# Optimization experiments

Measured on AMD Instinct MI355X. Metric: run time of the kernel, lower is better.

## Reference

```python
import jax, jax.numpy as jnp
import numpy as np

N, E = 20000, 320000
EPS = 1e-5
NEG_SLOPE = 0.2


def gat_conv(x, src, dst, W, att_src, att_dst, bias, num_nodes):
    # W: [Fin, H*C], att_*: [H, C], bias: [H*C]
    H, C = att_src.shape
    h = (x @ W).reshape(num_nodes, H, C)            # [N,H,C]
    a_s = jnp.einsum('nhc,hc->nh', h, att_src)      # [N,H]
    a_d = jnp.einsum('nhc,hc->nh', h, att_dst)      # [N,H]
    e = jax.nn.leaky_relu(a_s[src] + a_d[dst], NEG_SLOPE)  # [E,H]
    m = jax.ops.segment_max(e, dst, num_segments=num_nodes)       # per-dst max (self-loops guarantee non-empty)
    ex = jnp.exp(e - m[dst])
    s = jax.ops.segment_sum(ex, dst, num_segments=num_nodes)
    alpha = ex / s[dst]                              # [E,H] segment softmax
    out = jax.ops.segment_sum(h[src] * alpha[:, :, None], dst, num_segments=num_nodes)  # [N,H,C]
    return out.reshape(num_nodes, H * C) + bias


def batch_norm(x, gamma, beta):
    mu = x.mean(axis=0)
    var = x.var(axis=0)  # biased, as torch BN uses for normalization
    return (x - mu) * jax.lax.rsqrt(var + EPS) * gamma + beta


def setup_inputs() -> dict:
    key = jax.random.key(0)
    ks = jax.random.split(key, 32)
    x = jax.random.normal(ks[0], (N, 512), dtype=jnp.float32)
    edge_index = jax.random.randint(ks[1], (2, E), 0, N, dtype=jnp.int32)
    d = {"x": x, "edge_index": edge_index}
    # layer configs: (Fin, C_out, H)
    cfgs = [(512, 64, 8), (512, 64, 4), (256, 64, 2), (128, 16, 1)]
    i = 2
    for li, (fin, c, h) in enumerate(cfgs, start=1):
        sc = 1.0 / np.sqrt(fin)
        d[f"W{li}"] = jax.random.normal(ks[i], (fin, h * c), dtype=jnp.float32) * sc; i += 1
        d[f"as{li}"] = jax.random.normal(ks[i], (h, c), dtype=jnp.float32) * 0.1; i += 1
        d[f"ad{li}"] = jax.random.normal(ks[i], (h, c), dtype=jnp.float32) * 0.1; i += 1
        d[f"b{li}"] = jnp.zeros((h * c,), dtype=jnp.float32)
        if li < 4:
            d[f"g{li}"] = jnp.ones((h * c,), dtype=jnp.float32)
            d[f"be{li}"] = jnp.zeros((h * c,), dtype=jnp.float32)
    return d


def reference(x, edge_index, W1, as1, ad1, b1, g1, be1, W2, as2, ad2, b2, g2, be2, W3, as3, ad3, b3, g3, be3, W4, as4, ad4, b4):
    num_nodes = x.shape[0]
    loop = jnp.arange(num_nodes, dtype=edge_index.dtype)
    src = jnp.concatenate([edge_index[0], loop])  # add_self_loops=True
    dst = jnp.concatenate([edge_index[1], loop])
    h = gat_conv(x, src, dst, W1, as1, ad1, b1, num_nodes)
    h = jax.nn.elu(batch_norm(h, g1, be1))
    h = gat_conv(h, src, dst, W2, as2, ad2, b2, num_nodes)
    h = jax.nn.elu(batch_norm(h, g2, be2))
    h = gat_conv(h, src, dst, W3, as3, ad3, b3, num_nodes)
    h = jax.nn.elu(batch_norm(h, g3, be3))
    h = gat_conv(h, src, dst, W4, as4, ad4, b4, num_nodes)
    return jax.nn.log_softmax(h, axis=1)
```

## Files before the change

### kernel.cpp

```cpp
#include <hip/hip_runtime.h>
#include <hip/hip_bf16.h>
#include <cstdint>
#include <cstddef>

#define NN 20000
#define EE 320000
#define ET (EE + NN)
#define MPAD 20096
#define SCHUNK 20

typedef __attribute__((ext_vector_type(8))) short  short8;
typedef __attribute__((ext_vector_type(4))) float  floatx4;

__device__ inline unsigned short f2bf(float f) {
    unsigned u = __float_as_uint(f);
    u += 0x7FFFu + ((u >> 16) & 1u);
    return (unsigned short)(u >> 16);
}
__device__ inline float bf2f(unsigned short b) {
    return __uint_as_float(((unsigned)b) << 16);
}
__device__ inline float bflo(unsigned u) { return __uint_as_float(u << 16); }
__device__ inline float bfhi(unsigned u) { return __uint_as_float(u & 0xFFFF0000u); }

__global__ void zero_i32(int* __restrict__ p, int n) {
    int i = blockIdx.x * blockDim.x + threadIdx.x;
    if (i < n) p[i] = 0;
}

#define W1SZ (512 * 512)
#define W2SZ (512 * 256)
#define W3SZ (256 * 128)
#define NA_BLOCKS (MPAD * 512 / 4 / 256)
#define NW_BLOCKS ((W1SZ + W2SZ + W3SZ) / 256)
__global__ void prep_all(const float* __restrict__ x, unsigned short* __restrict__ bufA,
                         const float* __restrict__ W1, unsigned short* __restrict__ Wt1,
                         const float* __restrict__ W2, unsigned short* __restrict__ Wt2,
                         const float* __restrict__ W3, unsigned short* __restrict__ Wt3) {
    const int b = blockIdx.x;
    if (b < NA_BLOCKS) {
        long long base = ((long long)b * 256 + threadIdx.x) * 4;
        int row = (int)(base / 512);
        float4 v = make_float4(0.f, 0.f, 0.f, 0.f);
        if (row < NN) v = *(const float4*)(x + base);
        ushort4 o;
        o.x = f2bf(v.x); o.y = f2bf(v.y); o.z = f2bf(v.z); o.w = f2bf(v.w);
        *(ushort4*)(bufA + base) = o;
    } else {
        int i = (b - NA_BLOCKS) * 256 + threadIdx.x;
        const float* W; unsigned short* Wt; int K, N, idx;
        if (i < W1SZ)                    { W = W1; Wt = Wt1; K = 512; N = 512; idx = i; }
        else if (i < W1SZ + W2SZ)        { W = W2; Wt = Wt2; K = 512; N = 256; idx = i - W1SZ; }
        else                             { W = W3; Wt = Wt3; K = 256; N = 128; idx = i - W1SZ - W2SZ; }
        int k = idx / N, n = idx - k * N;
        Wt[(size_t)n * K + k] = f2bf(W[idx]);
    }
}

__global__ void count_edges(const int* __restrict__ dst, int* __restrict__ cnt) {
    int e = blockIdx.x * blockDim.x + threadIdx.x;
    if (e >= ET) return;
    int d = (e < EE) ? dst[e] : (e - EE);
    atomicAdd(&cnt[d], 1);
}

__global__ __launch_bounds__(1024) void scan_fast(const int* __restrict__ cnt,
                                                  int* __restrict__ rowp,
                                                  int* __restrict__ wptr, int n) {
    __shared__ int sums[1024];
    const int t = threadIdx.x;
    const int base = t * SCHUNK;
    int local[SCHUNK];
    int acc = 0;
#pragma unroll
    for (int i = 0; i < SCHUNK; ++i) {
        int idx = base + i;
        int v = (idx < n) ? cnt[idx] : 0;
        local[i] = acc;
        acc += v;
    }
    sums[t] = acc;
    __syncthreads();
    for (int o = 1; o < 1024; o <<= 1) {
        int u = (t >= o) ? sums[t - o] : 0;
        __syncthreads();
        sums[t] += u;
        __syncthreads();
    }
    int excl = sums[t] - acc;
#pragma unroll
    for (int i = 0; i < SCHUNK; ++i) {
        int idx = base + i;
        if (idx < n) { int rp = excl + local[i]; rowp[idx] = rp; wptr[idx] = rp; }
    }
    if (t == 1023) rowp[n] = sums[1023];
}

__global__ void fill_edges(const int* __restrict__ src, const int* __restrict__ dst,
                           int* __restrict__ wptr, int* __restrict__ colx) {
    int e = blockIdx.x * blockDim.x + threadIdx.x;
    if (e >= ET) return;
    int s, d;
    if (e < EE) { s = src[e]; d = dst[e]; } else { s = e - EE; d = e - EE; }
    int pos = atomicAdd(&wptr[d], 1);
    colx[pos] = s;
}

template <bool BN>
__global__ __launch_bounds__(256) void gemm_bf16_fused(
        const void* __restrict__ Av, const unsigned short* __restrict__ Bt,
        unsigned short* __restrict__ hN, float* __restrict__ aS, float* __restrict__ aD,
        const float* __restrict__ atts, const float* __restrict__ attd,
        const float* __restrict__ ssg,
        int M, int N, int K, int Mreal) {
    __shared__ unsigned short As[128][40];
    __shared__ unsigned short Bs[128][40];
    __shared__ float ssS[512];
    __shared__ float ssH[512];
    const int t = threadIdx.x;
    const int lane = t & 63, wave = t >> 6;
    const int wm = wave >> 1, wn = wave & 1;
    const int quad = lane >> 4, mrow = lane & 15;
    const int row0 = blockIdx.y * 128, col0 = blockIdx.x * 128;
    const int srow = t >> 2, schunk = (t & 3) * 8;

    if (BN) {
        for (int i = t; i < K; i += 256) { ssS[i] = ssg[i]; ssH[i] = ssg[K + i]; }
        __syncthreads();
    }

    floatx4 acc[4][4];
#pragma unroll
    for (int i = 0; i < 4; ++i)
#pragma unroll
        for (int j = 0; j < 4; ++j)
#pragma unroll
            for (int r = 0; r < 4; ++r) acc[i][j][r] = 0.f;

    for (int k0 = 0; k0 < K; k0 += 32) {
        uint4 ra0, ra1;
        if constexpr (!BN) {
            const unsigned short* A = (const unsigned short*)Av;
            ra0 = *(const uint4*)(A + (size_t)(row0 + srow)      * K + k0 + schunk);
            ra1 = *(const uint4*)(A + (size_t)(row0 + srow + 64) * K + k0 + schunk);
        } else {
            const float* A = (const float*)Av;
            float sc[8], sh[8];
#pragma unroll
            for (int i = 0; i < 8; ++i) { sc[i] = ssS[k0 + schunk + i]; sh[i] = ssH[k0 + schunk + i]; }
            auto stage_row = [&](int arow) -> uint4 {
                uint4 r = make_uint4(0u, 0u, 0u, 0u);
                if (arow < Mreal) {
                    float4 f0 = *(const float4*)(A + (size_t)arow * K + k0 + schunk);
                    float4 f1 = *(const float4*)(A + (size_t)arow * K + k0 + schunk + 4);
                    float v[8] = { f0.x, f0.y, f0.z, f0.w, f1.x, f1.y, f1.z, f1.w };
                    unsigned short h[8];
#pragma unroll
                    for (int i = 0; i < 8; ++i) {
                        float u = v[i] * sc[i] + sh[i];
                        u = (u > 0.f) ? u : (__expf(u) - 1.f);
                        h[i] = f2bf(u);
                    }
                    r = make_uint4((unsigned)h[0] | ((unsigned)h[1] << 16),
                                   (unsigned)h[2] | ((unsigned)h[3] << 16),
                                   (unsigned)h[4] | ((unsigned)h[5] << 16),
                                   (unsigned)h[6] | ((unsigned)h[7] << 16));
                }
                return r;
            };
            ra0 = stage_row(row0 + srow);
            ra1 = stage_row(row0 + srow + 64);
        }
        uint4 rb0 = *(const uint4*)(Bt + (size_t)(col0 + srow)      * K + k0 + schunk);
        uint4 rb1 = *(const uint4*)(Bt + (size_t)(col0 + srow + 64) * K + k0 + schunk);
        __syncthreads();
        *(uint4*)&As[srow][schunk]      = ra0;
        *(uint4*)&As[srow + 64][schunk] = ra1;
        *(uint4*)&Bs[srow][schunk]      = rb0;
        *(uint4*)&Bs[srow + 64][schunk] = rb1;
        __syncthreads();

        short8 af[4], bfr[4];
#pragma unroll
        for (int i = 0; i < 4; ++i)
            af[i] = *(const short8*)&As[wm * 64 + i * 16 + mrow][quad * 8];
#pragma unroll
        for (int j = 0; j < 4; ++j)
            bfr[j] = *(const short8*)&Bs[wn * 64 + j * 16 + mrow][quad * 8];
#pragma unroll
        for (int i = 0; i < 4; ++i)
#pragma unroll
            for (int j = 0; j < 4; ++j)
                acc[i][j] = __builtin_amdgcn_mfma_f32_16x16x32_bf16(af[i], bfr[j], acc[i][j], 0, 0, 0);
    }

    const int head = (col0 + wn * 64) >> 6;
    float attS[4], attD[4];
#pragma unroll
    for (int j = 0; j < 4; ++j) {
        attS[j] = atts[head * 64 + j * 16 + mrow];
        attD[j] = attd[head * 64 + j * 16 + mrow];
    }

#pragma unroll
    for (int i = 0; i < 4; ++i) {
#pragma unroll
        for (int r = 0; r < 4; ++r) {
            int row = row0 + wm * 64 + i * 16 + quad * 4 + r;
            float ps = acc[i][0][r] * attS[0] + acc[i][1][r] * attS[1]
                     + acc[i][2][r] * attS[2] + acc[i][3][r] * attS[3];
            float pd = acc[i][0][r] * attD[0] + acc[i][1][r] * attD[1]
                     + acc[i][2][r] * attD[2] + acc[i][3][r] * attD[3];
#pragma unroll
            for (int o = 1; o < 16; o <<= 1) {
                ps += __shfl_xor(ps, o);
                pd += __shfl_xor(pd, o);
            }
            if (row < M) {
                if (mrow == 0) {
                    aS[(size_t)head * M + row] = ps;
                    aD[(size_t)head * M + row] = pd;
                }
#pragma unroll
                for (int j = 0; j < 4; ++j)
                    hN[(size_t)row * N + col0 + wn * 64 + j * 16 + mrow] = f2bf(acc[i][j][r]);
            }
        }
    }
}

template <int HH>
__global__ __launch_bounds__(256) void gat_agg_head32(
        const unsigned short* __restrict__ hN,
        const float* __restrict__ aS, const float* __restrict__ aD,
        const int* __restrict__ rowp, const int* __restrict__ colx,
        const float* __restrict__ bias, float* __restrict__ out,
        float* __restrict__ part, int Nn) {
    constexpr int F = HH * 64;
    constexpr unsigned F2 = F * 2;
    constexpr int G = 8 / HH;
    __shared__ uint2 pair[4][4][33];
    __shared__ float red[4][16][9];
    const int L = blockIdx.x;
    const int x8 = L & 7;
    const int hd = x8 / G;
    const int nodeblk = (L >> 3) * G + (x8 & (G - 1));
    const int wave = threadIdx.x >> 6, lane = threadIdx.x & 63;
    const int grp = lane >> 4;
    const int q   = lane & 15;
    const int eo  = q >> 3;
    const int lo  = (q & 7) * 16;
    const int n = nodeblk * 16 + wave * 4 + grp;
    const bool valid = (n < Nn);

    const char* hb = (const char*)hN + hd * 128;

    float a0 = 0.f, a1 = 0.f, a2 = 0.f, a3 = 0.f;
    float a4 = 0.f, a5 = 0.f, a6 = 0.f, a7 = 0.f;
    float4 o4 = make_float4(0.f, 0.f, 0.f, 0.f);

    if (valid) {
        const float* aSh = aS + (size_t)hd * Nn;
        const float adv = aD[(size_t)hd * Nn + n];
        const int b0 = rowp[n], b1 = rowp[n + 1];

        float m, s;

        auto gather = [&](int cnt) {
            for (int j = 0; j < cnt; j += 8) {
                uint2 x0 = pair[wave][grp][j + eo + 0];
                uint2 x1 = pair[wave][grp][j + eo + 2];
                uint2 x2 = pair[wave][grp][j + eo + 4];
                uint2 x3 = pair[wave][grp][j + eo + 6];
                uint4 v0 = *(const uint4*)(hb + x0.x + lo);
                uint4 v1 = *(const uint4*)(hb + x1.x + lo);
                uint4 v2 = *(const uint4*)(hb + x2.x + lo);
                uint4 v3 = *(const uint4*)(hb + x3.x + lo);
                float p0 = __uint_as_float(x0.y), p1 = __uint_as_float(x1.y);
                float p2 = __uint_as_float(x2.y), p3 = __uint_as_float(x3.y);
                a0 += p0 * bflo(v0.x) + p1 * bflo(v1.x) + p2 * bflo(v2.x) + p3 * bflo(v3.x);
                a1 += p0 * bfhi(v0.x) + p1 * bfhi(v1.x) + p2 * bfhi(v2.x) + p3 * bfhi(v3.x);
                a2 += p0 * bflo(v0.y) + p1 * bflo(v1.y) + p2 * bflo(v2.y) + p3 * bflo(v3.y);
                a3 += p0 * bfhi(v0.y) + p1 * bfhi(v1.y) + p2 * bfhi(v2.y) + p3 * bfhi(v3.y);
                a4 += p0 * bflo(v0.z) + p1 * bflo(v1.z) + p2 * bflo(v2.z) + p3 * bflo(v3.z);
                a5 += p0 * bfhi(v0.z) + p1 * bfhi(v1.z) + p2 * bfhi(v2.z) + p3 * bfhi(v3.z);
                a6 += p0 * bflo(v0.w) + p1 * bflo(v1.w) + p2 * bflo(v2.w) + p3 * bflo(v3.w);
                a7 += p0 * bfhi(v0.w) + p1 * bfhi(v1.w) + p2 * bfhi(v2.w) + p3 * bfhi(v3.w);
            }
        };

        {
            const int cnt = min(32, b1 - b0);
            int sn0 = 0, sn1 = 0;
            if (q < cnt)      sn0 = colx[b0 + q];
            if (q + 16 < cnt) sn1 = colx[b0 + q + 16];
            float t0 = aSh[sn0] + adv;
            float t1 = aSh[sn1] + adv;
            float e0 = (q < cnt)      ? ((t0 > 0.f) ? t0 : 0.2f * t0) : -1e30f;
            float e1 = (q + 16 < cnt) ? ((t1 > 0.f) ? t1 : 0.2f * t1) : -1e30f;
            float mc = fmaxf(e0, e1);
#pragma unroll
            for (int o = 8; o > 0; o >>= 1) mc = fmaxf(mc, __shfl_xor(mc, o));
            m = mc;
            float p0 = __expf(e0 - m);
            float p1 = __expf(e1 - m);
            float ps = p0 + p1;
#pragma unroll
            for (int o = 8; o > 0; o >>= 1) ps += __shfl_xor(ps, o);
            s = ps;
            pair[wave][grp][q]      = make_uint2((unsigned)sn0 * F2, __float_as_uint(p0));
            pair[wave][grp][q + 16] = make_uint2((unsigned)sn1 * F2, __float_as_uint(p1));
            __threadfence_block();
            gather(cnt);
        }

        for (int c0 = b0 + 32; c0 < b1; c0 += 32) {
            __threadfence_block();
            const int cnt = min(32, b1 - c0);
            int sn0 = 0, sn1 = 0;
            if (q < cnt)      sn0 = colx[c0 + q];
            if (q + 16 < cnt) sn1 = colx[c0 + q + 16];
            float t0 = aSh[sn0] + adv;
            float t1 = aSh[sn1] + adv;
            float e0 = (q < cnt)      ? ((t0 > 0.f) ? t0 : 0.2f * t0) : -1e30f;
            float e1 = (q + 16 < cnt) ? ((t1 > 0.f) ? t1 : 0.2f * t1) : -1e30f;
            float mc = fmaxf(e0, e1);
#pragma unroll
            for (int o = 8; o > 0; o >>= 1) mc = fmaxf(mc, __shfl_xor(mc, o));
            float nm = fmaxf(m, mc);
            float sc = __expf(m - nm);
            float p0 = __expf(e0 - nm);
            float p1 = __expf(e1 - nm);
            float ps = p0 + p1;
#pragma unroll
            for (int o = 8; o > 0; o >>= 1) ps += __shfl_xor(ps, o);
            s = s * sc + ps;
            a0 *= sc; a1 *= sc; a2 *= sc; a3 *= sc;
            a4 *= sc; a5 *= sc; a6 *= sc; a7 *= sc;
            m = nm;
            pair[wave][grp][q]      = make_uint2((unsigned)sn0 * F2, __float_as_uint(p0));
            pair[wave][grp][q + 16] = make_uint2((unsigned)sn1 * F2, __float_as_uint(p1));
            __threadfence_block();
            gather(cnt);
        }

        a0 += __shfl_xor(a0, 8); a1 += __shfl_xor(a1, 8);
        a2 += __shfl_xor(a2, 8); a3 += __shfl_xor(a3, 8);
        a4 += __shfl_xor(a4, 8); a5 += __shfl_xor(a5, 8);
        a6 += __shfl_xor(a6, 8); a7 += __shfl_xor(a7, 8);

        const float inv = 1.f / s;
        float r0 = eo ? a4 : a0;
        float r1 = eo ? a5 : a1;
        float r2 = eo ? a6 : a2;
        float r3 = eo ? a7 : a3;
        const int cb = hd * 64 + (q & 7) * 8 + eo * 4;
        o4.x = r0 * inv + bias[cb + 0];
        o4.y = r1 * inv + bias[cb + 1];
        o4.z = r2 * inv + bias[cb + 2];
        o4.w = r3 * inv + bias[cb + 3];
        *(float4*)(out + (size_t)n * F + cb) = o4;
    }

    float s0 = o4.x, s1 = o4.y, s2 = o4.z, s3 = o4.w;
    float q0 = s0 * s0, q1 = s1 * s1, q2 = s2 * s2, q3 = s3 * s3;
#pragma unroll
    for (int o = 16; o < 64; o <<= 1) {
        s0 += __shfl_xor(s0, o); s1 += __shfl_xor(s1, o);
        s2 += __shfl_xor(s2, o); s3 += __shfl_xor(s3, o);
        q0 += __shfl_xor(q0, o); q1 += __shfl_xor(q1, o);
        q2 += __shfl_xor(q2, o); q3 += __shfl_xor(q3, o);
    }
    if (grp == 0) {
        red[wave][q][0] = s0; red[wave][q][1] = s1;
        red[wave][q][2] = s2; red[wave][q][3] = s3;
        red[wave][q][4] = q0; red[wave][q][5] = q1;
        red[wave][q][6] = q2; red[wave][q][7] = q3;
    }
    __syncthreads();
    if (wave == 0 && lane < 16) {
        float a[8];
#pragma unroll
        for (int k = 0; k < 8; ++k)
            a[k] = red[0][q][k] + red[1][q][k] + red[2][q][k] + red[3][q][k];
        const int cq = (q & 7) * 2 + eo;
        float* pb = part + (size_t)L * 128;
#pragma unroll
        for (int k = 0; k < 4; ++k) {
            pb[cq * 4 + k]      = a[k];
            pb[64 + cq * 4 + k] = a[4 + k];
        }
    }
}

__global__ __launch_bounds__(256) void gemm_l4_fused(const float* __restrict__ A,
                                                     const float* __restrict__ B,
                                                     unsigned short* __restrict__ C,
                                                     float* __restrict__ aS, float* __restrict__ aD,
                                                     const float* __restrict__ atts,
                                                     const float* __restrict__ attd,
                                                     const float* __restrict__ ssg,
                                                     int M, int N, int K, int Mreal) {
    __shared__ float As[16][65];
    __shared__ float Bs[16][64];
    const int tid = threadIdx.x;
    const int tx = tid & 15, ty = tid >> 4;
    const int row0 = blockIdx.y * 64, col0 = blockIdx.x * 64;
    const int rA = tid >> 2, kq = (tid & 3) << 2;
    const int rB = tid >> 4, cq = (tid & 15) << 2;
    float acc[4][4] = {};

    for (int k0 = 0; k0 < K; k0 += 16) {
        const int arow = row0 + rA;
        float a0v = 0.f, a1v = 0.f, a2v = 0.f, a3v = 0.f;
        if (arow < Mreal) {
            float4 fa = *(const float4*)(A + (size_t)arow * K + k0 + kq);
            const int c = k0 + kq;
            a0v = fa.x * ssg[c + 0] + ssg[K + c + 0];
            a1v = fa.y * ssg[c + 1] + ssg[K + c + 1];
            a2v = fa.z * ssg[c + 2] + ssg[K + c + 2];
            a3v = fa.w * ssg[c + 3] + ssg[K + c + 3];
            a0v = (a0v > 0.f) ? a0v : (__expf(a0v) - 1.f);
            a1v = (a1v > 0.f) ? a1v : (__expf(a1v) - 1.f);
            a2v = (a2v > 0.f) ? a2v : (__expf(a2v) - 1.f);
            a3v = (a3v > 0.f) ? a3v : (__expf(a3v) - 1.f);
        }
        float4 fb = make_float4(0.f, 0.f, 0.f, 0.f);
        int bcol = col0 + cq;
        if (bcol < N) fb = *(const float4*)(B + (size_t)(k0 + rB) * N + bcol);
        As[kq + 0][rA] = a0v; As[kq + 1][rA] = a1v;
        As[kq + 2][rA] = a2v; As[kq + 3][rA] = a3v;
        *(float4*)&Bs[rB][cq] = fb;
        __syncthreads();
#pragma unroll
        for (int k = 0; k < 16; ++k) {
            float a0 = As[k][ty * 4 + 0];
            float a1 = As[k][ty * 4 + 1];
            float a2 = As[k][ty * 4 + 2];
            float a3 = As[k][ty * 4 + 3];
            float4 b = *(float4*)&Bs[k][tx * 4];
            acc[0][0] += a0 * b.x; acc[0][1] += a0 * b.y; acc[0][2] += a0 * b.z; acc[0][3] += a0 * b.w;
            acc[1][0] += a1 * b.x; acc[1][1] += a1 * b.y; acc[1][2] += a1 * b.z; acc[1][3] += a1 * b.w;
            acc[2][0] += a2 * b.x; acc[2][1] += a2 * b.y; acc[2][2] += a2 * b.z; acc[2][3] += a2 * b.w;
            acc[3][0] += a3 * b.x; acc[3][1] += a3 * b.y; acc[3][2] += a3 * b.z; acc[3][3] += a3 * b.w;
        }
        __syncthreads();
    }
    float as_part[4], ad_part[4];
#pragma unroll
    for (int i = 0; i < 4; ++i) { as_part[i] = 0.f; ad_part[i] = 0.f; }
    if (tx < 4) {
#pragma unroll
        for (int i = 0; i < 4; ++i) {
#pragma unroll
            for (int jj = 0; jj < 4; ++jj) {
                int c = tx * 4 + jj;
                as_part[i] += acc[i][jj] * atts[c];
                ad_part[i] += acc[i][jj] * attd[c];
            }
        }
    }
#pragma unroll
    for (int i = 0; i < 4; ++i) {
        float ps = as_part[i], pd = ad_part[i];
        ps += __shfl_xor(ps, 1); ps += __shfl_xor(ps, 2);
        pd += __shfl_xor(pd, 1); pd += __shfl_xor(pd, 2);
        int r = row0 + ty * 4 + i;
        if (r < M) {
            if (tx == 0) { aS[r] = ps; aD[r] = pd; }
#pragma unroll
            for (int jj = 0; jj < 4; ++jj) {
                int c = col0 + tx * 4 + jj;
                if (c < N) C[(size_t)r * N + c] = f2bf(acc[i][jj]);
            }
        }
    }
}

template <int C>
__global__ void gat_agg_l4_ls(const unsigned short* __restrict__ ht,
                              const float* __restrict__ as, const float* __restrict__ aD,
                              const int* __restrict__ rowp, const int* __restrict__ colx,
                              const float* __restrict__ bias, float* __restrict__ out, int Nn) {
    int n = blockIdx.x * 4 + (threadIdx.x >> 6);
    int lane = threadIdx.x & 63;
    if (n >= Nn) return;
    float adv = aD[n];
    int b0 = rowp[n], b1 = rowp[n + 1];

    float m = -1e30f, s = 0.f, acc = 0.f;
    for (int c0 = b0; c0 < b1; c0 += 64) {
        int cnt = b1 - c0; if (cnt > 64) cnt = 64;
        int sn = 0; float e = -1e30f;
        if (lane < cnt) {
            sn = colx[c0 + lane];
            float tt = as[sn] + adv;
            e = (tt > 0.f) ? tt : 0.2f * tt;
        }
        float mc = e;
#pragma unroll
        for (int o = 32; o > 0; o >>= 1) mc = fmaxf(mc, __shfl_xor(mc, o));
        float nm = fmaxf(m, mc);
        float sc = __expf(m - nm);
        acc *= sc; s *= sc;
        float p = (lane < cnt) ? __expf(e - nm) : 0.f;
        float ps = p;
#pragma unroll
        for (int o = 32; o > 0; o >>= 1) ps += __shfl_xor(ps, o);
        s += ps; m = nm;

        int j = 0;
        for (; j + 4 <= cnt; j += 4) {
            int s0 = __shfl(sn, j),     s1 = __shfl(sn, j + 1);
            int s2 = __shfl(sn, j + 2), s3 = __shfl(sn, j + 3);
            float p0 = __shfl(p, j),     p1 = __shfl(p, j + 1);
            float p2 = __shfl(p, j + 2), p3 = __shfl(p, j + 3);
            float h0 = 0.f, h1 = 0.f, h2 = 0.f, h3 = 0.f;
            if (lane < C) {
                h0 = bf2f(ht[(size_t)s0 * C + lane]);
                h1 = bf2f(ht[(size_t)s1 * C + lane]);
                h2 = bf2f(ht[(size_t)s2 * C + lane]);
                h3 = bf2f(ht[(size_t)s3 * C + lane]);
            }
            acc += p0 * h0 + p1 * h1 + p2 * h2 + p3 * h3;
        }
        for (; j < cnt; ++j) {
            int sj = __shfl(sn, j);
            float pj = __shfl(p, j);
            float hv = (lane < C) ? bf2f(ht[(size_t)sj * C + lane]) : 0.f;
            acc += pj * hv;
        }
    }
    float v = (lane < C) ? (acc / s + bias[lane]) : -1e30f;
    float mx = v;
#pragma unroll
    for (int o = 8; o > 0; o >>= 1) mx = fmaxf(mx, __shfl_xor(mx, o));
    float ex = (lane < C) ? __expf(v - mx) : 0.f;
#pragma unroll
    for (int o = 8; o > 0; o >>= 1) ex += __shfl_xor(ex, o);
    float l = __logf(ex) + mx;
    if (lane < C) out[(size_t)n * C + lane] = v - l;
}

template <int F>
__global__ __launch_bounds__(1024) void bn_reduce_par(const float* __restrict__ part,
                                                      const float* __restrict__ gamma,
                                                      const float* __restrict__ beta,
                                                      float* __restrict__ ss,
                                                      float invN, int NB8) {
    constexpr int G = 512 / F;
    __shared__ float sd[32][33];
    const int t = threadIdx.x;
    const int pr = t >> 5;
    const int tg = t & 31;
    const int c0 = blockIdx.x * 16;
    const int c  = c0 + (tg & 15);
    const int hd = c >> 6;
    const int off = (c & 63) + ((tg < 16) ? 0 : 64);
    float a0 = 0.f, a1 = 0.f, a2 = 0.f, a3 = 0.f;
    for (int g = 0; g < G; ++g) {
        const float* pb = part + (size_t)(hd * G + g) * 128 + off;
        int j = pr;
        for (; j + 96 < NB8; j += 128) {
            a0 += pb[(size_t)(j +  0) * 1024];
            a1 += pb[(size_t)(j + 32) * 1024];
            a2 += pb[(size_t)(j + 64) * 1024];
            a3 += pb[(size_t)(j + 96) * 1024];
        }
        for (; j < NB8; j += 32)
            a0 += pb[(size_t)j * 1024];
    }
    sd[pr][tg] = (a0 + a1) + (a2 + a3);
    __syncthreads();
    if (pr == 0) {
        float tot = sd[0][tg];
#pragma unroll
        for (int r = 1; r < 32; ++r) tot += sd[r][tg];
        sd[0][tg] = tot;
    }
    __syncthreads();
    if (t < 16) {
        int cc = c0 + t;
        float s = sd[0][t];
        float q = sd[0][16 + t];
        float mu = s * invN;
        float var = q * invN - mu * mu;
        float sc = gamma[cc] * rsqrtf(var + 1e-5f);
        ss[cc] = sc;
        ss[F + cc] = beta[cc] - mu * sc;
    }
}

extern "C" void kernel_launch(void* const* d_in, const int* in_sizes, int n_in,
                              void* d_out, int out_size, void* d_ws, size_t ws_size,
                              hipStream_t stream) {
    const float* x   = (const float*)d_in[0];
    const int*   ei  = (const int*)d_in[1];
    const float* W1  = (const float*)d_in[2];
    const float* as1 = (const float*)d_in[3];
    const float* ad1 = (const float*)d_in[4];
    const float* b1  = (const float*)d_in[5];
    const float* ga1 = (const float*)d_in[6];
    const float* be1 = (const float*)d_in[7];
    const float* W2  = (const float*)d_in[8];
    const float* as2 = (const float*)d_in[9];
    const float* ad2 = (const float*)d_in[10];
    const float* b2  = (const float*)d_in[11];
    const float* ga2 = (const float*)d_in[12];
    const float* be2 = (const float*)d_in[13];
    const float* W3  = (const float*)d_in[14];
    const float* as3 = (const float*)d_in[15];
    const float* ad3 = (const float*)d_in[16];
    const float* b3  = (const float*)d_in[17];
    const float* ga3 = (const float*)d_in[18];
    const float* be3 = (const float*)d_in[19];
    const float* W4  = (const float*)d_in[20];
    const float* as4 = (const float*)d_in[21];
    const float* ad4 = (const float*)d_in[22];
    const float* b4  = (const float*)d_in[23];
    float* outp = (float*)d_out;

    uint8_t* base = (uint8_t*)d_ws;
    size_t off = 0;
    auto alloc = [&](size_t nbytes) -> void* {
        off = (off + 255) & ~(size_t)255;
        void* p = base + off;
        off += nbytes;
        return p;
    };
    float* bufO = (float*)alloc((size_t)NN * 512 * 4);
    unsigned short* bufA = (unsigned short*)alloc((size_t)MPAD * 512 * 2);
    unsigned short* hN   = (unsigned short*)alloc((size_t)NN * 512 * 2);
    unsigned short* Wt1  = (unsigned short*)alloc((size_t)512 * 512 * 2);
    unsigned short* Wt2  = (unsigned short*)alloc((size_t)256 * 512 * 2);
    unsigned short* Wt3  = (unsigned short*)alloc((size_t)128 * 256 * 2);
    float* aSn  = (float*)alloc((size_t)NN * 8 * 4);
    float* aDn  = (float*)alloc((size_t)NN * 8 * 4);
    int*   cnt  = (int*)alloc((size_t)NN * 4);
    int*   rowp = (int*)alloc((size_t)(NN + 1) * 4);
    int*   wptr = (int*)alloc((size_t)NN * 4);
    int*   colx = (int*)alloc((size_t)ET * 4);
    float* bnp  = (float*)alloc((size_t)10048 * 128 * 4);
    float* bns  = (float*)alloc((size_t)1024 * 4);

    const int* srcRow = ei;
    const int* dstRow = ei + EE;

    zero_i32<<<(NN + 255) / 256, 256, 0, stream>>>(cnt, NN);
    count_edges<<<(ET + 255) / 256, 256, 0, stream>>>(dstRow, cnt);
    scan_fast<<<1, 1024, 0, stream>>>(cnt, rowp, wptr, NN);
    fill_edges<<<(ET + 255) / 256, 256, 0, stream>>>(srcRow, dstRow, wptr, colx);

    prep_all<<<NA_BLOCKS + NW_BLOCKS, 256, 0, stream>>>(x, bufA, W1, Wt1, W2, Wt2, W3, Wt3);

    const int NBLK = (NN + 15) / 16;

    {
        dim3 g(512 / 128, MPAD / 128);
        gemm_bf16_fused<false><<<g, 256, 0, stream>>>(bufA, Wt1, hN, aSn, aDn, as1, ad1,
                                                      nullptr, NN, 512, 512, 0);
        gat_agg_head32<8><<<NBLK * 8, 256, 0, stream>>>(hN, aSn, aDn, rowp, colx, b1, bufO, bnp, NN);
        bn_reduce_par<512><<<512 / 16, 1024, 0, stream>>>(bnp, ga1, be1, bns, 1.0f / NN, NBLK);
    }
    {
        dim3 g(256 / 128, MPAD / 128);
        gemm_bf16_fused<true><<<g, 256, 0, stream>>>(bufO, Wt2, hN, aSn, aDn, as2, ad2,
                                                     bns, NN, 256, 512, NN);
        const int nb8 = (NBLK + 1) / 2;
        gat_agg_head32<4><<<nb8 * 8, 256, 0, stream>>>(hN, aSn, aDn, rowp, colx, b2, bufO, bnp, NN);
        bn_reduce_par<256><<<256 / 16, 1024, 0, stream>>>(bnp, ga2, be2, bns, 1.0f / NN, nb8);
    }
    {
        dim3 g(128 / 128, MPAD / 128);
        gemm_bf16_fused<true><<<g, 256, 0, stream>>>(bufO, Wt3, hN, aSn, aDn, as3, ad3,
                                                     bns, NN, 128, 256, NN);
        const int nb8 = (NBLK + 3) / 4;
        gat_agg_head32<2><<<nb8 * 8, 256, 0, stream>>>(hN, aSn, aDn, rowp, colx, b3, bufO, bnp, NN);
        bn_reduce_par<128><<<128 / 16, 1024, 0, stream>>>(bnp, ga3, be3, bns, 1.0f / NN, nb8);
    }
    {
        dim3 g(1, (NN + 63) / 64);
        gemm_l4_fused<<<g, 256, 0, stream>>>(bufO, W4, hN, aSn, aDn, as4, ad4,
                                             bns, NN, 16, 128, NN);
        gat_agg_l4_ls<16><<<(NN + 3) / 4, 256, 0, stream>>>(hN, aSn, aDn, rowp, colx, b4, outp, NN);
    }
}
```

Measured before the change: 397.9 us.

## Fuse fp32-to-bf16 input conversion into GEMM and remap block indices for XCD locality

Drops the separate pass that converted x to a padded bf16 buffer. The first-layer GEMM now reads fp32 x directly and converts while staging tiles, which removes a full write and re-read of a 20k×512 bf16 buffer. The GEMM grid also becomes 1D with a swizzled block-to-tile mapping, where the low 3 bits pick the row group, presumably so blocks sharing A rows land on the same XCD/L2. Launches are padded to 160 row tiles and blocks beyond 157 exit early. The trade-off is that layer 1 reads twice as many A bytes (fp32) from global memory in each K step.

```diff
diff --git a/kernel.cpp b/kernel.cpp
--- a/kernel.cpp
+++ b/kernel.cpp
@@ -31,30 +31,18 @@
 #define W1SZ (512 * 512)
 #define W2SZ (512 * 256)
 #define W3SZ (256 * 128)
-#define NA_BLOCKS (MPAD * 512 / 4 / 256)
 #define NW_BLOCKS ((W1SZ + W2SZ + W3SZ) / 256)
-__global__ void prep_all(const float* __restrict__ x, unsigned short* __restrict__ bufA,
-                         const float* __restrict__ W1, unsigned short* __restrict__ Wt1,
-                         const float* __restrict__ W2, unsigned short* __restrict__ Wt2,
-                         const float* __restrict__ W3, unsigned short* __restrict__ Wt3) {
-    const int b = blockIdx.x;
-    if (b < NA_BLOCKS) {
-        long long base = ((long long)b * 256 + threadIdx.x) * 4;
-        int row = (int)(base / 512);
-        float4 v = make_float4(0.f, 0.f, 0.f, 0.f);
-        if (row < NN) v = *(const float4*)(x + base);
-        ushort4 o;
-        o.x = f2bf(v.x); o.y = f2bf(v.y); o.z = f2bf(v.z); o.w = f2bf(v.w);
-        *(ushort4*)(bufA + base) = o;
-    } else {
-        int i = (b - NA_BLOCKS) * 256 + threadIdx.x;
-        const float* W; unsigned short* Wt; int K, N, idx;
-        if (i < W1SZ)                    { W = W1; Wt = Wt1; K = 512; N = 512; idx = i; }
-        else if (i < W1SZ + W2SZ)        { W = W2; Wt = Wt2; K = 512; N = 256; idx = i - W1SZ; }
-        else                             { W = W3; Wt = Wt3; K = 256; N = 128; idx = i - W1SZ - W2SZ; }
-        int k = idx / N, n = idx - k * N;
-        Wt[(size_t)n * K + k] = f2bf(W[idx]);
-    }
+__global__ void cvt_w_all(const float* __restrict__ W1, unsigned short* __restrict__ Wt1,
+                          const float* __restrict__ W2, unsigned short* __restrict__ Wt2,
+                          const float* __restrict__ W3, unsigned short* __restrict__ Wt3) {
+    int i = blockIdx.x * blockDim.x + threadIdx.x;
+    const float* W; unsigned short* Wt; int K, N, idx;
+    if (i < W1SZ)                    { W = W1; Wt = Wt1; K = 512; N = 512; idx = i; }
+    else if (i < W1SZ + W2SZ)        { W = W2; Wt = Wt2; K = 512; N = 256; idx = i - W1SZ; }
+    else if (i < W1SZ + W2SZ + W3SZ) { W = W3; Wt = Wt3; K = 256; N = 128; idx = i - W1SZ - W2SZ; }
+    else return;
+    int k = idx / N, n = idx - k * N;
+    Wt[(size_t)n * K + k] = f2bf(W[idx]);
 }
 
 __global__ void count_edges(const int* __restrict__ dst, int* __restrict__ cnt) {
@@ -106,25 +94,32 @@
     colx[pos] = s;
 }
 
-template <bool BN>
+template <int MODE>
 __global__ __launch_bounds__(256) void gemm_bf16_fused(
-        const void* __restrict__ Av, const unsigned short* __restrict__ Bt,
+        const float* __restrict__ A, const unsigned short* __restrict__ Bt,
         unsigned short* __restrict__ hN, float* __restrict__ aS, float* __restrict__ aD,
         const float* __restrict__ atts, const float* __restrict__ attd,
         const float* __restrict__ ssg,
-        int M, int N, int K, int Mreal) {
+        int M, int N, int K, int Mreal, int gxsh, int gy) {
     __shared__ unsigned short As[128][40];
     __shared__ unsigned short Bs[128][40];
     __shared__ float ssS[512];
     __shared__ float ssH[512];
+
+    const int lid = blockIdx.x;
+    const int c8 = lid & 7, kk = lid >> 3;
+    const int bx = kk & ((1 << gxsh) - 1);
+    const int by = c8 + 8 * (kk >> gxsh);
+    if (by >= gy) return;
+
     const int t = threadIdx.x;
     const int lane = t & 63, wave = t >> 6;
     const int wm = wave >> 1, wn = wave & 1;
     const int quad = lane >> 4, mrow = lane & 15;
-    const int row0 = blockIdx.y * 128, col0 = blockIdx.x * 128;
+    const int row0 = by * 128, col0 = bx * 128;
     const int srow = t >> 2, schunk = (t & 3) * 8;
 
-    if (BN) {
+    if constexpr (MODE == 2) {
         for (int i = t; i < K; i += 256) { ssS[i] = ssg[i]; ssH[i] = ssg[K + i]; }
         __syncthreads();
     }
@@ -138,39 +133,36 @@
             for (int r = 0; r < 4; ++r) acc[i][j][r] = 0.f;
 
     for (int k0 = 0; k0 < K; k0 += 32) {
-        uint4 ra0, ra1;
-        if constexpr (!BN) {
-            const unsigned short* A = (const unsigned short*)Av;
-            ra0 = *(const uint4*)(A + (size_t)(row0 + srow)      * K + k0 + schunk);
-            ra1 = *(const uint4*)(A + (size_t)(row0 + srow + 64) * K + k0 + schunk);
-        } else {
-            const float* A = (const float*)Av;
-            float sc[8], sh[8];
+        float sc[8], sh[8];
+        if constexpr (MODE == 2) {
 #pragma unroll
             for (int i = 0; i < 8; ++i) { sc[i] = ssS[k0 + schunk + i]; sh[i] = ssH[k0 + schunk + i]; }
-            auto stage_row = [&](int arow) -> uint4 {
-                uint4 r = make_uint4(0u, 0u, 0u, 0u);
-                if (arow < Mreal) {
-                    float4 f0 = *(const float4*)(A + (size_t)arow * K + k0 + schunk);
-                    float4 f1 = *(const float4*)(A + (size_t)arow * K + k0 + schunk + 4);
-                    float v[8] = { f0.x, f0.y, f0.z, f0.w, f1.x, f1.y, f1.z, f1.w };
-                    unsigned short h[8];
-#pragma unroll
-                    for (int i = 0; i < 8; ++i) {
-                        float u = v[i] * sc[i] + sh[i];
+        }
+        auto stage_row = [&](int arow) -> uint4 {
+            uint4 r = make_uint4(0u, 0u, 0u, 0u);
+            if (arow < Mreal) {
+                float4 f0 = *(const float4*)(A + (size_t)arow * K + k0 + schunk);
+                float4 f1 = *(const float4*)(A + (size_t)arow * K + k0 + schunk + 4);
+                float v[8] = { f0.x, f0.y, f0.z, f0.w, f1.x, f1.y, f1.z, f1.w };
+                unsigned short h[8];
+#pragma unroll
+                for (int i = 0; i < 8; ++i) {
+                    float u = v[i];
+                    if constexpr (MODE == 2) {
+                        u = u * sc[i] + sh[i];
                         u = (u > 0.f) ? u : (__expf(u) - 1.f);
-                        h[i] = f2bf(u);
                     }
-                    r = make_uint4((unsigned)h[0] | ((unsigned)h[1] << 16),
-                                   (unsigned)h[2] | ((unsigned)h[3] << 16),
-                                   (unsigned)h[4] | ((unsigned)h[5] << 16),
-                                   (unsigned)h[6] | ((unsigned)h[7] << 16));
+                    h[i] = f2bf(u);
                 }
-                return r;
-            };
-            ra0 = stage_row(row0 + srow);
-            ra1 = stage_row(row0 + srow + 64);
-        }
+                r = make_uint4((unsigned)h[0] | ((unsigned)h[1] << 16),
+                               (unsigned)h[2] | ((unsigned)h[3] << 16),
+                               (unsigned)h[4] | ((unsigned)h[5] << 16),
+                               (unsigned)h[6] | ((unsigned)h[7] << 16));
+            }
+            return r;
+        };
+        uint4 ra0 = stage_row(row0 + srow);
+        uint4 ra1 = stage_row(row0 + srow + 64);
         uint4 rb0 = *(const uint4*)(Bt + (size_t)(col0 + srow)      * K + k0 + schunk);
         uint4 rb1 = *(const uint4*)(Bt + (size_t)(col0 + srow + 64) * K + k0 + schunk);
         __syncthreads();
@@ -629,7 +621,6 @@
         return p;
     };
     float* bufO = (float*)alloc((size_t)NN * 512 * 4);
-    unsigned short* bufA = (unsigned short*)alloc((size_t)MPAD * 512 * 2);
     unsigned short* hN   = (unsigned short*)alloc((size_t)NN * 512 * 2);
     unsigned short* Wt1  = (unsigned short*)alloc((size_t)512 * 512 * 2);
     unsigned short* Wt2  = (unsigned short*)alloc((size_t)256 * 512 * 2);
@@ -651,29 +642,27 @@
     scan_fast<<<1, 1024, 0, stream>>>(cnt, rowp, wptr, NN);
     fill_edges<<<(ET + 255) / 256, 256, 0, stream>>>(srcRow, dstRow, wptr, colx);
 
-    prep_all<<<NA_BLOCKS + NW_BLOCKS, 256, 0, stream>>>(x, bufA, W1, Wt1, W2, Wt2, W3, Wt3);
+    cvt_w_all<<<NW_BLOCKS, 256, 0, stream>>>(W1, Wt1, W2, Wt2, W3, Wt3);
 
     const int NBLK = (NN + 15) / 16;
+    const int GY8 = 160;
 
     {
-        dim3 g(512 / 128, MPAD / 128);
-        gemm_bf16_fused<false><<<g, 256, 0, stream>>>(bufA, Wt1, hN, aSn, aDn, as1, ad1,
-                                                      nullptr, NN, 512, 512, 0);
+        gemm_bf16_fused<1><<<4 * GY8, 256, 0, stream>>>(x, Wt1, hN, aSn, aDn, as1, ad1,
+                                                        nullptr, NN, 512, 512, NN, 2, 157);
         gat_agg_head32<8><<<NBLK * 8, 256, 0, stream>>>(hN, aSn, aDn, rowp, colx, b1, bufO, bnp, NN);
         bn_reduce_par<512><<<512 / 16, 1024, 0, stream>>>(bnp, ga1, be1, bns, 1.0f / NN, NBLK);
     }
     {
-        dim3 g(256 / 128, MPAD / 128);
-        gemm_bf16_fused<true><<<g, 256, 0, stream>>>(bufO, Wt2, hN, aSn, aDn, as2, ad2,
-                                                     bns, NN, 256, 512, NN);
+        gemm_bf16_fused<2><<<2 * GY8, 256, 0, stream>>>(bufO, Wt2, hN, aSn, aDn, as2, ad2,
+                                                        bns, NN, 256, 512, NN, 1, 157);
         const int nb8 = (NBLK + 1) / 2;
         gat_agg_head32<4><<<nb8 * 8, 256, 0, stream>>>(hN, aSn, aDn, rowp, colx, b2, bufO, bnp, NN);
         bn_reduce_par<256><<<256 / 16, 1024, 0, stream>>>(bnp, ga2, be2, bns, 1.0f / NN, nb8);
     }
     {
-        dim3 g(128 / 128, MPAD / 128);
-        gemm_bf16_fused<true><<<g, 256, 0, stream>>>(bufO, Wt3, hN, aSn, aDn, as3, ad3,
-                                                     bns, NN, 128, 256, NN);
+        gemm_bf16_fused<2><<<1 * GY8, 256, 0, stream>>>(bufO, Wt3, hN, aSn, aDn, as3, ad3,
+                                                        bns, NN, 128, 256, NN, 0, 157);
         const int nb8 = (NBLK + 3) / 4;
         gat_agg_head32<2><<<nb8 * 8, 256, 0, stream>>>(hN, aSn, aDn, rowp, colx, b3, bufO, bnp, NN);
         bn_reduce_par<128><<<128 / 16, 1024, 0, stream>>>(bnp, ga3, be3, bns, 1.0f / NN, nb8);
```

Result: no change. 401.0 us (+0.8%).
